# Kernel tuning notes

Measured on AMD Instinct MI355X. Metric: run time of the kernel, lower is better.

Reference implementation:

```python
import jax, jax.numpy as jnp
import numpy as np


def setup_inputs() -> dict:
    key = jax.random.key(0)
    kx, kw = jax.random.split(key)
    B, D, H, W, K = 32, 128, 64, 64, 1024
    x = jax.random.normal(kx, (B, D, H, W), dtype=jnp.float32)
    # matches torch init: uniform(-1/k, 1/k), shape (d, k)
    weight = jax.random.uniform(kw, (D, K), dtype=jnp.float32,
                                minval=-1.0 / K, maxval=1.0 / K)
    return {"x": x, "weight": weight}


def reference(x, weight):
    # x: [B, d, H, W], weight (codebook emb): [d, k]
    # argmin of L2 norm == argmin of squared distance:
    x2 = jnp.sum(x * x, axis=1)                      # [B, H, W]
    e2 = jnp.sum(weight * weight, axis=0)            # [k]
    xe = jnp.einsum('bdhw,dk->bhwk', x, weight)      # [B, H, W, k]
    d2 = x2[..., None] - 2.0 * xe + e2               # [B, H, W, k]
    argmin = jnp.argmin(d2, axis=-1)                 # [B, H, W] int
    # gather codebook rows then move channel dim back to axis 1
    result = jnp.take(weight.T, argmin, axis=0)      # [B, H, W, d]
    result = jnp.transpose(result, (0, 3, 1, 2))     # [B, d, H, W]
    return result, argmin
```

## Files before the change

### kernel.cpp

```cpp
#include <hip/hip_runtime.h>
#include <math.h>

#define DD   128
#define KK   1024
#define HWW  4096
#define NPIX 131072
#define EPS  1.5e-4f
#define CAPA 32768
#define CAPB 8192

#define WS_WT    0
#define WS_E2    131072
#define WS_CTR   132096
#define WS_LISTA 132160
#define WS_LISTB 230464
#define WS_BHI   246848
#define WS_BLO   312384

typedef short  short8  __attribute__((ext_vector_type(8)));
typedef float  floatx4 __attribute__((ext_vector_type(4)));

static __device__ __forceinline__ unsigned short f2bf(float x) {
    unsigned u = __float_as_uint(x);
    return (unsigned short)((u + 0x7fffu + ((u >> 16) & 1u)) >> 16);
}
static __device__ __forceinline__ float bf2f(unsigned short b) {
    return __uint_as_float(((unsigned)b) << 16);
}

__global__ __launch_bounds__(256) void prep_all(
        const float* __restrict__ w,
        float* __restrict__ wT, float* __restrict__ e2,
        short8* __restrict__ bhi, short8* __restrict__ blo,
        int* __restrict__ ctr) {
    int t = blockIdx.x * 256 + threadIdx.x;
    if (t < 32768) {
        int k = t & 1023, d4 = t >> 10;
        float4 v;
        v.x = w[(d4 * 4 + 0) * KK + k];
        v.y = w[(d4 * 4 + 1) * KK + k];
        v.z = w[(d4 * 4 + 2) * KK + k];
        v.w = w[(d4 * 4 + 3) * KK + k];
        *(float4*)(wT + (size_t)k * DD + d4 * 4) = v;
    } else if (t < 49152) {
        int u     = t - 32768;
        int lane  = u & 63;
        int chunk = (u >> 6) & 3;
        int ktile = u >> 8;
        int kcol  = ktile * 16 + (lane & 15);
        int d0    = chunk * 32 + (lane >> 4) * 8;
        short8 h, l;
#pragma unroll
        for (int j = 0; j < 8; ++j) {
            float wv = w[(size_t)(d0 + j) * KK + kcol];
            unsigned short hb = f2bf(wv);
            h[j] = (short)hb;
            l[j] = (short)f2bf(wv - bf2f(hb));
        }
        bhi[u] = h;
        blo[u] = l;
    } else if (t < 50176) {
        int k = t - 49152;
        if (k == 0) { ctr[0] = 0; ctr[1] = 0; }
        float acc = 0.0f;
        for (int d = 0; d < DD; ++d) {
            float v = w[d * KK + k];
            acc = __fadd_rn(acc, __fmul_rn(v, v));
        }
        e2[k] = acc;
    }
}

__global__ __launch_bounds__(256) void vq_screen(
        const float* __restrict__ x,
        const float* __restrict__ wT,
        const float* __restrict__ e2,
        const short8* __restrict__ bhi,
        const short8* __restrict__ blo,
        float* __restrict__ out,
        int* __restrict__ listA,
        int* __restrict__ listB,
        int* __restrict__ ctr) {
    __shared__ int sk1[4][32];

    const int tid  = threadIdx.x;
    const int wave = tid >> 6;
    const int lane = tid & 63;
    const int q    = lane >> 4;
    const int col  = lane & 15;

    const int b       = blockIdx.x >> 5;
    const int base_hw = (blockIdx.x & 31) * 128 + wave * 32;

    short8 a0h[4], a0l[4], a1h[4], a1l[4];
#pragma unroll
    for (int c = 0; c < 4; ++c) {
#pragma unroll
        for (int j = 0; j < 8; ++j) {
            int d = c * 32 + q * 8 + j;
            const float* xr = x + (size_t)(b * DD + d) * HWW + base_hw;
            float x0 = xr[col];
            float x1 = xr[16 + col];
            unsigned short h0 = f2bf(x0), h1 = f2bf(x1);
            a0h[c][j] = (short)h0;  a0l[c][j] = (short)f2bf(x0 - bf2f(h0));
            a1h[c][j] = (short)h1;  a1l[c][j] = (short)f2bf(x1 - bf2f(h1));
        }
    }

    float s1[8], s2[8], s3[8];
    int   c1[8], c2[8];
    float prevS[8];
    float prevE2 = 0.0f;
#pragma unroll
    for (int i = 0; i < 8; ++i) {
        s1[i] = INFINITY; s2[i] = INFINITY; s3[i] = INFINITY;
        c1[i] = 0; c2[i] = 0;
        prevS[i] = -INFINITY;
    }

    auto top3_update = [&](int ktile) {
        const int kcur = ktile * 16 + col;
#pragma unroll
        for (int i = 0; i < 8; ++i) {
            float s = fmaf(-2.0f, prevS[i], prevE2);
            bool lt1 = s < s1[i];
            bool lt2 = s < s2[i];
            s3[i] = __builtin_amdgcn_fmed3f(s, s2[i], s3[i]);
            s2[i] = __builtin_amdgcn_fmed3f(s, s1[i], s2[i]);
            c2[i] = lt1 ? c1[i] : (lt2 ? kcur : c2[i]);
            s1[i] = fminf(s, s1[i]);
            c1[i] = lt1 ? kcur : c1[i];
        }
    };

    const short8* pbh = bhi + lane;
    const short8* pbl = blo + lane;

    short8 hA0, hA1, hA2, hA3, lA0, lA1, lA2, lA3;
    short8 hB0, hB1, hB2, hB3, lB0, lB1, lB2, lB3;

    hA0 = pbh[0];   hA1 = pbh[64];  hA2 = pbh[128]; hA3 = pbh[192];
    lA0 = pbl[0];   lA1 = pbl[64];  lA2 = pbl[128]; lA3 = pbl[192];

#define MFMA_TILE(H0, H1, H2, H3, L0, L1, L2, L3)                              \
    {                                                                          \
        floatx4 p00 = {0.f,0.f,0.f,0.f}, p01 = {0.f,0.f,0.f,0.f};              \
        floatx4 p10 = {0.f,0.f,0.f,0.f}, p11 = {0.f,0.f,0.f,0.f};              \
        p00 = __builtin_amdgcn_mfma_f32_16x16x32_bf16(a0h[0], H0, p00, 0,0,0); \
        p01 = __builtin_amdgcn_mfma_f32_16x16x32_bf16(a0h[1], H1, p01, 0,0,0); \
        p00 = __builtin_amdgcn_mfma_f32_16x16x32_bf16(a0h[2], H2, p00, 0,0,0); \
        p01 = __builtin_amdgcn_mfma_f32_16x16x32_bf16(a0h[3], H3, p01, 0,0,0); \
        p00 = __builtin_amdgcn_mfma_f32_16x16x32_bf16(a0h[0], L0, p00, 0,0,0); \
        p01 = __builtin_amdgcn_mfma_f32_16x16x32_bf16(a0h[1], L1, p01, 0,0,0); \
        p00 = __builtin_amdgcn_mfma_f32_16x16x32_bf16(a0h[2], L2, p00, 0,0,0); \
        p01 = __builtin_amdgcn_mfma_f32_16x16x32_bf16(a0h[3], L3, p01, 0,0,0); \
        p00 = __builtin_amdgcn_mfma_f32_16x16x32_bf16(a0l[0], H0, p00, 0,0,0); \
        p01 = __builtin_amdgcn_mfma_f32_16x16x32_bf16(a0l[1], H1, p01, 0,0,0); \
        p00 = __builtin_amdgcn_mfma_f32_16x16x32_bf16(a0l[2], H2, p00, 0,0,0); \
        p01 = __builtin_amdgcn_mfma_f32_16x16x32_bf16(a0l[3], H3, p01, 0,0,0); \
        p10 = __builtin_amdgcn_mfma_f32_16x16x32_bf16(a1h[0], H0, p10, 0,0,0); \
        p11 = __builtin_amdgcn_mfma_f32_16x16x32_bf16(a1h[1], H1, p11, 0,0,0); \
        p10 = __builtin_amdgcn_mfma_f32_16x16x32_bf16(a1h[2], H2, p10, 0,0,0); \
        p11 = __builtin_amdgcn_mfma_f32_16x16x32_bf16(a1h[3], H3, p11, 0,0,0); \
        p10 = __builtin_amdgcn_mfma_f32_16x16x32_bf16(a1h[0], L0, p10, 0,0,0); \
        p11 = __builtin_amdgcn_mfma_f32_16x16x32_bf16(a1h[1], L1, p11, 0,0,0); \
        p10 = __builtin_amdgcn_mfma_f32_16x16x32_bf16(a1h[2], L2, p10, 0,0,0); \
        p11 = __builtin_amdgcn_mfma_f32_16x16x32_bf16(a1h[3], L3, p11, 0,0,0); \
        p10 = __builtin_amdgcn_mfma_f32_16x16x32_bf16(a1l[0], H0, p10, 0,0,0); \
        p11 = __builtin_amdgcn_mfma_f32_16x16x32_bf16(a1l[1], H1, p11, 0,0,0); \
        p10 = __builtin_amdgcn_mfma_f32_16x16x32_bf16(a1l[2], H2, p10, 0,0,0); \
        p11 = __builtin_amdgcn_mfma_f32_16x16x32_bf16(a1l[3], H3, p11, 0,0,0); \
        prevS[0] = p00[0] + p01[0];                                            \
        prevS[1] = p00[1] + p01[1];                                            \
        prevS[2] = p00[2] + p01[2];                                            \
        prevS[3] = p00[3] + p01[3];                                            \
        prevS[4] = p10[0] + p11[0];                                            \
        prevS[5] = p10[1] + p11[1];                                            \
        prevS[6] = p10[2] + p11[2];                                            \
        prevS[7] = p10[3] + p11[3];                                            \
        prevE2   = e2v;                                                        \
    }

    for (int kt = 0; kt < 64; kt += 2) {
        {
            const int nb = (kt + 1) * 256;
            hB0 = pbh[nb];       hB1 = pbh[nb + 64];
            hB2 = pbh[nb + 128]; hB3 = pbh[nb + 192];
            lB0 = pbl[nb];       lB1 = pbl[nb + 64];
            lB2 = pbl[nb + 128]; lB3 = pbl[nb + 192];
            float e2v = e2[kt * 16 + col];
            top3_update(kt - 1);
            MFMA_TILE(hA0, hA1, hA2, hA3, lA0, lA1, lA2, lA3)
        }
        {
            const int nb = ((kt + 2) & 63) * 256;
            hA0 = pbh[nb];       hA1 = pbh[nb + 64];
            hA2 = pbh[nb + 128]; hA3 = pbh[nb + 192];
            lA0 = pbl[nb];       lA1 = pbl[nb + 64];
            lA2 = pbl[nb + 128]; lA3 = pbl[nb + 192];
            float e2v = e2[(kt + 1) * 16 + col];
            top3_update(kt);
            MFMA_TILE(hB0, hB1, hB2, hB3, lB0, lB1, lB2, lB3)
        }
    }
    top3_update(63);
#undef MFMA_TILE

#pragma unroll
    for (int off = 1; off < 16; off <<= 1) {
#pragma unroll
        for (int i = 0; i < 8; ++i) {
            float o1 = __shfl_xor(s1[i], off);
            float o2 = __shfl_xor(s2[i], off);
            float o3 = __shfl_xor(s3[i], off);
            int   ok1 = __shfl_xor(c1[i], off);
            int   ok2 = __shfl_xor(c2[i], off);
            bool afirst = (s1[i] < o1) || (s1[i] == o1 && c1[i] < ok1);
            float n1, n2, n3; int nk1, nk2;
            if (afirst) {
                bool asec = (s2[i] < o1) || (s2[i] == o1 && c2[i] < ok1);
                n1 = s1[i]; nk1 = c1[i];
                n2 = asec ? s2[i] : o1;  nk2 = asec ? c2[i] : ok1;
                n3 = asec ? fminf(s3[i], o1) : fminf(s2[i], o2);
            } else {
                bool bsec = (o2 < s1[i]) || (o2 == s1[i] && ok2 < c1[i]);
                n1 = o1; nk1 = ok1;
                n2 = bsec ? o2 : s1[i];  nk2 = bsec ? ok2 : c1[i];
                n3 = bsec ? fminf(o3, s1[i]) : fminf(o2, s2[i]);
            }
            s1[i] = n1; s2[i] = n2; s3[i] = n3; c1[i] = nk1; c2[i] = nk2;
        }
    }

#pragma unroll
    for (int g = 0; g < 2; ++g) {
#pragma unroll
        for (int r = 0; r < 4; ++r) {
            if (col == r) {
                const int i = g * 4 + r;
                int plocal = g * 16 + q * 4 + r;
                int hwp    = base_hw + plocal;
                int Pg     = b * HWW + hwp;
                out[(size_t)DD * NPIX + Pg] = (float)c1[i];
                sk1[wave][plocal] = c1[i];
                float g12 = s2[i] - s1[i];
                float g13 = s3[i] - s1[i];
                if (g12 <= EPS) {
                    if (g13 > EPS) {
                        int idx = atomicAdd(&ctr[0], 1);
                        if (idx < CAPA) {
                            listA[3 * idx + 0] = Pg;
                            listA[3 * idx + 1] = c1[i];
                            listA[3 * idx + 2] = c2[i];
                        }
                    } else {
                        int idx = atomicAdd(&ctr[1], 1);
                        if (idx < CAPB) listB[idx] = Pg;
                    }
                }
            }
        }
    }
    __syncthreads();

    {
        const int p_lo = lane & 15;
        const int dgrp = lane >> 4;
#pragma unroll
        for (int half = 0; half < 2; ++half) {
            const int plocal = half * 16 + p_lo;
            const int kk     = sk1[wave][plocal];
            const int hwp    = base_hw + plocal;
            const float* wrow = wT + (size_t)kk * DD;
#pragma unroll
            for (int i = 0; i < 32; ++i) {
                int d = i * 4 + dgrp;
                out[(size_t)(b * DD + d) * HWW + hwp] = wrow[d];
            }
        }
    }
}

__global__ __launch_bounds__(256) void vq_resolve(
        const float* __restrict__ x,
        const float* __restrict__ wT,
        const float* __restrict__ e2,
        const int* __restrict__ listA,
        const int* __restrict__ listB,
        const int* __restrict__ ctr,
        float* __restrict__ out) {
    const int nA = min(ctr[0], CAPA);
    const int nB = min(ctr[1], CAPB);
    const int tid  = threadIdx.x;
    const int gtid = blockIdx.x * 256 + tid;
    const int wave = gtid >> 6;
    const int lane = tid & 63;
    const int NW = (gridDim.x * 256) >> 6;
    const int NT = gridDim.x * 256;

    for (int j = wave; j < nB; j += NW) {
        const int p  = listB[j];
        const int b  = p >> 12;
        const int hw = p & (HWW - 1);
        const float* xp = x + (size_t)b * DD * HWW + hw;
        float xv[DD];
#pragma unroll 4
        for (int d = 0; d < DD; ++d) xv[d] = xp[(size_t)d * HWW];
        float x2 = 0.0f;
#pragma unroll 4
        for (int d = 0; d < DD; ++d) x2 = __fadd_rn(x2, __fmul_rn(xv[d], xv[d]));

        unsigned long long best = ~0ull;
        for (int kk = 0; kk < 16; ++kk) {
            const int k = lane * 16 + kk;
            const float* wk = wT + (size_t)k * DD;
            float a = 0.0f;
#pragma unroll 4
            for (int d = 0; d < DD; ++d)
                a = __fadd_rn(a, __fmul_rn(xv[d], wk[d]));
            float d2 = __fadd_rn(__fsub_rn(x2, 2.0f * a), e2[k]);
            unsigned long long c =
                ((unsigned long long)__float_as_uint(d2) << 32) | (unsigned)k;
            best = best < c ? best : c;
        }
#pragma unroll
        for (int off = 32; off; off >>= 1) {
            unsigned long long o = __shfl_xor(best, off);
            best = best < o ? best : o;
        }
        const int kwin = (int)(best & 0xffffffffu);
        if (lane == 0) out[(size_t)DD * NPIX + p] = (float)kwin;
        const float* wb = wT + (size_t)kwin * DD;
        float* op = out + (size_t)b * DD * HWW + hw;
        op[(size_t)lane * HWW]        = wb[lane];
        op[(size_t)(lane + 64) * HWW] = wb[lane + 64];
    }

    for (int i = blockIdx.x + tid * gridDim.x; i < nA; i += NT) {
        const int p  = listA[3 * i + 0];
        const int kA = listA[3 * i + 1];
        const int kB = listA[3 * i + 2];
        const int b  = p >> 12;
        const int hw = p & (HWW - 1);
        const float* xp = x + (size_t)b * DD * HWW + hw;
        const float* wa = wT + (size_t)kA * DD;
        const float* wb = wT + (size_t)kB * DD;
        float x2 = 0.0f, aa = 0.0f, ab = 0.0f;
#pragma unroll 4
        for (int d = 0; d < DD; ++d) {
            float xd = xp[(size_t)d * HWW];
            x2 = __fadd_rn(x2, __fmul_rn(xd, xd));
            aa = __fadd_rn(aa, __fmul_rn(xd, wa[d]));
            ab = __fadd_rn(ab, __fmul_rn(xd, wb[d]));
        }
        float dA = __fadd_rn(__fsub_rn(x2, 2.0f * aa), e2[kA]);
        float dB = __fadd_rn(__fsub_rn(x2, 2.0f * ab), e2[kB]);
        const int kwin = (dA < dB || (dA == dB && kA < kB)) ? kA : kB;
        out[(size_t)DD * NPIX + p] = (float)kwin;
        const float* ww = wT + (size_t)kwin * DD;
        float* op = out + (size_t)b * DD * HWW + hw;
#pragma unroll 8
        for (int d = 0; d < DD; ++d) op[(size_t)d * HWW] = ww[d];
    }
}

extern "C" void kernel_launch(void* const* d_in, const int* in_sizes, int n_in,
                              void* d_out, int out_size, void* d_ws, size_t ws_size,
                              hipStream_t stream) {
    const float* x = (const float*)d_in[0];
    const float* w = (const float*)d_in[1];
    float* out = (float*)d_out;
    float* wsf = (float*)d_ws;

    float*  wT    = wsf + WS_WT;
    float*  e2    = wsf + WS_E2;
    int*    ctr   = (int*)(wsf + WS_CTR);
    int*    listA = (int*)(wsf + WS_LISTA);
    int*    listB = (int*)(wsf + WS_LISTB);
    short8* bhi   = (short8*)(wsf + WS_BHI);
    short8* blo   = (short8*)(wsf + WS_BLO);

    prep_all  <<<dim3(196),  dim3(256), 0, stream>>>(w, wT, e2, bhi, blo, ctr);
    vq_screen <<<dim3(1024), dim3(256), 0, stream>>>(x, wT, e2, bhi, blo, out,
                                                     listA, listB, ctr);
    vq_resolve<<<dim3(256),  dim3(256), 0, stream>>>(x, wT, e2, listA, listB,
                                                     ctr, out);
}
```

Baseline: 444.1 us.

## Split resolve kernel into scan and pair kernels, skip rewrites when argmin unchanged

Splits the fallback resolve pass into two kernels: a full-codebook scan for ambiguous pixels, now launched with fewer blocks, and a two-candidate pair check. The scan stages each pixel's 128-dim vector in shared memory instead of a 128-float register array, which cuts register pressure. Both kernels skip rewriting the index and gathered codebook row when the exact winner matches the screen's guess, saving strided global writes. The cost is an extra launch, and the scan now depends on the screen kernel having already written its guess into the output.

Result: faster. 377.8 us (-14.9%).

```diff
diff --git a/kernel.cpp b/kernel.cpp
--- a/kernel.cpp
+++ b/kernel.cpp
@@ -281,34 +281,35 @@
     }
 }
 
-__global__ __launch_bounds__(256) void vq_resolve(
+__global__ __launch_bounds__(256) void vq_scan(
         const float* __restrict__ x,
         const float* __restrict__ wT,
         const float* __restrict__ e2,
-        const int* __restrict__ listA,
         const int* __restrict__ listB,
         const int* __restrict__ ctr,
         float* __restrict__ out) {
-    const int nA = min(ctr[0], CAPA);
+    __shared__ float sxv[4][DD];
     const int nB = min(ctr[1], CAPB);
-    const int tid  = threadIdx.x;
-    const int gtid = blockIdx.x * 256 + tid;
-    const int wave = gtid >> 6;
-    const int lane = tid & 63;
-    const int NW = (gridDim.x * 256) >> 6;
-    const int NT = gridDim.x * 256;
+    const int tid   = threadIdx.x;
+    const int lane  = tid & 63;
+    const int lwave = tid >> 6;
+    const int wave  = (blockIdx.x * 256 + tid) >> 6;
+    const int NW    = (gridDim.x * 256) >> 6;
 
     for (int j = wave; j < nB; j += NW) {
         const int p  = listB[j];
         const int b  = p >> 12;
         const int hw = p & (HWW - 1);
         const float* xp = x + (size_t)b * DD * HWW + hw;
-        float xv[DD];
-#pragma unroll 4
-        for (int d = 0; d < DD; ++d) xv[d] = xp[(size_t)d * HWW];
+
+        sxv[lwave][lane]      = xp[(size_t)lane * HWW];
+        sxv[lwave][lane + 64] = xp[(size_t)(lane + 64) * HWW];
+        __builtin_amdgcn_wave_barrier();
+
+        const float* xv = sxv[lwave];
         float x2 = 0.0f;
-#pragma unroll 4
-        for (int d = 0; d < DD; ++d) x2 = __fadd_rn(x2, __fmul_rn(xv[d], xv[d]));
+        for (int d = 0; d < DD; ++d)
+            x2 = __fadd_rn(x2, __fmul_rn(xv[d], xv[d]));
 
         unsigned long long best = ~0ull;
         for (int kk = 0; kk < 16; ++kk) {
@@ -328,13 +329,29 @@
             unsigned long long o = __shfl_xor(best, off);
             best = best < o ? best : o;
         }
-        const int kwin = (int)(best & 0xffffffffu);
-        if (lane == 0) out[(size_t)DD * NPIX + p] = (float)kwin;
-        const float* wb = wT + (size_t)kwin * DD;
-        float* op = out + (size_t)b * DD * HWW + hw;
-        op[(size_t)lane * HWW]        = wb[lane];
-        op[(size_t)(lane + 64) * HWW] = wb[lane + 64];
-    }
+        const int kwin  = (int)(best & 0xffffffffu);
+        const int guess = (int)out[(size_t)DD * NPIX + p];
+        if (kwin != guess) {
+            if (lane == 0) out[(size_t)DD * NPIX + p] = (float)kwin;
+            const float* wb = wT + (size_t)kwin * DD;
+            float* op = out + (size_t)b * DD * HWW + hw;
+            op[(size_t)lane * HWW]        = wb[lane];
+            op[(size_t)(lane + 64) * HWW] = wb[lane + 64];
+        }
+        __builtin_amdgcn_wave_barrier();
+    }
+}
+
+__global__ __launch_bounds__(256) void vq_pair(
+        const float* __restrict__ x,
+        const float* __restrict__ wT,
+        const float* __restrict__ e2,
+        const int* __restrict__ listA,
+        const int* __restrict__ ctr,
+        float* __restrict__ out) {
+    const int nA = min(ctr[0], CAPA);
+    const int tid = threadIdx.x;
+    const int NT  = gridDim.x * 256;
 
     for (int i = blockIdx.x + tid * gridDim.x; i < nA; i += NT) {
         const int p  = listA[3 * i + 0];
@@ -356,11 +373,13 @@
         float dA = __fadd_rn(__fsub_rn(x2, 2.0f * aa), e2[kA]);
         float dB = __fadd_rn(__fsub_rn(x2, 2.0f * ab), e2[kB]);
         const int kwin = (dA < dB || (dA == dB && kA < kB)) ? kA : kB;
-        out[(size_t)DD * NPIX + p] = (float)kwin;
-        const float* ww = wT + (size_t)kwin * DD;
-        float* op = out + (size_t)b * DD * HWW + hw;
+        if (kwin != kA) {
+            out[(size_t)DD * NPIX + p] = (float)kwin;
+            const float* ww = wT + (size_t)kwin * DD;
+            float* op = out + (size_t)b * DD * HWW + hw;
 #pragma unroll 8
-        for (int d = 0; d < DD; ++d) op[(size_t)d * HWW] = ww[d];
+            for (int d = 0; d < DD; ++d) op[(size_t)d * HWW] = ww[d];
+        }
     }
 }
 
@@ -380,9 +399,9 @@
     short8* bhi   = (short8*)(wsf + WS_BHI);
     short8* blo   = (short8*)(wsf + WS_BLO);
 
-    prep_all  <<<dim3(196),  dim3(256), 0, stream>>>(w, wT, e2, bhi, blo, ctr);
-    vq_screen <<<dim3(1024), dim3(256), 0, stream>>>(x, wT, e2, bhi, blo, out,
-                                                     listA, listB, ctr);
-    vq_resolve<<<dim3(256),  dim3(256), 0, stream>>>(x, wT, e2, listA, listB,
-                                                     ctr, out);
-}
+    prep_all <<<dim3(196),  dim3(256), 0, stream>>>(w, wT, e2, bhi, blo, ctr);
+    vq_screen<<<dim3(1024), dim3(256), 0, stream>>>(x, wT, e2, bhi, blo, out,
+                                                    listA, listB, ctr);
+    vq_scan  <<<dim3(64),   dim3(256), 0, stream>>>(x, wT, e2, listB, ctr, out);
+    vq_pair  <<<dim3(256),  dim3(256), 0, stream>>>(x, wT, e2, listA, ctr, out);
+}
```
